# Optimization experiments

Hardware: AMD Instinct MI355X
Metric: run time of the kernel (lower is better)

## Reference

```python
import jax, jax.numpy as jnp
from jax import lax
import numpy as np

WIN_SIZE = 11
WIN_SIGMA = 1.5
DATA_RANGE = 1.0
K1, K2 = 0.01, 0.03
DN = ('NCHW', 'OIHW', 'NCHW')


def _gauss_1d(size, sigma):
    coords = jnp.arange(size, dtype=jnp.float32) - (size // 2)
    g = jnp.exp(-coords ** 2 / (2.0 * sigma ** 2))
    return g / g.sum()


def _gaussian_filter(x, g):
    # depthwise separable valid conv: along W then along H (order irrelevant)
    C = x.shape[1]
    kw = jnp.tile(g.reshape(1, 1, 1, -1), (C, 1, 1, 1))  # [C,1,1,K]
    kh = jnp.tile(g.reshape(1, 1, -1, 1), (C, 1, 1, 1))  # [C,1,K,1]
    x = lax.conv_general_dilated(x, kw, (1, 1), 'VALID',
                                 feature_group_count=C, dimension_numbers=DN)
    x = lax.conv_general_dilated(x, kh, (1, 1), 'VALID',
                                 feature_group_count=C, dimension_numbers=DN)
    return x


def setup_inputs() -> dict:
    key = jax.random.key(0)
    k1, k2 = jax.random.split(key)
    X = jax.random.uniform(k1, (32, 3, 512, 512), dtype=jnp.float32, minval=-1.0, maxval=1.0)
    Y = jax.random.uniform(k2, (32, 3, 512, 512), dtype=jnp.float32, minval=-1.0, maxval=1.0)
    return {"X": X, "Y": Y}


def reference(X, Y):
    # channel == 3 -> normalize from [-1,1] to [0,1]
    X = (X + 1.0) / 2.0
    Y = (Y + 1.0) / 2.0

    g = _gauss_1d(WIN_SIZE, WIN_SIGMA).astype(X.dtype)
    C1 = (K1 * DATA_RANGE) ** 2
    C2 = (K2 * DATA_RANGE) ** 2

    mu1 = _gaussian_filter(X, g)
    mu2 = _gaussian_filter(Y, g)
    mu1_sq = mu1 * mu1
    mu2_sq = mu2 * mu2
    mu1_mu2 = mu1 * mu2

    sigma1_sq = _gaussian_filter(X * X, g) - mu1_sq
    sigma2_sq = _gaussian_filter(Y * Y, g) - mu2_sq
    sigma12 = _gaussian_filter(X * Y, g) - mu1_mu2

    cs_map = (2.0 * sigma12 + C2) / (sigma1_sq + sigma2_sq + C2)
    ssim_map = (2.0 * mu1_mu2 + C1) / (mu1_sq + mu2_sq + C1) * cs_map

    # size_average=True, full=False -> scalar mean SSIM
    return ssim_map.mean()
```

## Files before the change

### kernel.cpp

```cpp
#include <hip/hip_runtime.h>
#include <cmath>


#define HH 512
#define WW 512
#define OH 502
#define OW 502
#define NC 96
#define TXS 32
#define BROWS 32
#define NIT 16
#define RAWR 64
#define RAWP 13
#define HSR 48
#define HP4 33
#define GX 16
#define NSLOT 64

typedef float f4 __attribute__((ext_vector_type(4)));

struct GaussW { float g[11]; };

static __device__ __forceinline__ f4 sp(float s) { return (f4){s, s, s, s}; }

#define FENCE() asm volatile("" ::: "memory")

__global__ __launch_bounds__(256, 4) void ssim_kernel(
        const float* __restrict__ X, const float* __restrict__ Y,
        double* __restrict__ acc, GaussW gw) {
    __shared__ f4 rawS[2 * RAWR * RAWP];
    __shared__ f4 hS[HSR][HP4];
    __shared__ double wsum[4];

    const int tid = threadIdx.x;
    const int C0 = blockIdx.x * TXS;
    const float* Xp = X + (size_t)blockIdx.y * (HH * WW);
    const float* Yp = Y + (size_t)blockIdx.y * (HH * WW);

    auto dma1 = [&](int a, int slot_f4, int row, int c4) {
        const float* bp  = a ? Yp : Xp;
        const float* src = bp + (size_t)min(row, HH - 1) * WW
                              + min(C0 + 4 * c4, WW - 4);
        f4* dst = rawS + a * (RAWR * RAWP) + slot_f4;
        __builtin_amdgcn_global_load_lds(
            (const __attribute__((address_space(1))) void*)src,
            (__attribute__((address_space(3))) void*)dst, 16, 0, 0);
    };

    auto dma_batch = [&](int i) {
        const int half = (i & 1) * (BROWS * RAWP);
        const int br = 32 * i + 42;
        #pragma unroll
        for (int a = 0; a < 2; ++a)
            #pragma unroll
            for (int k = 0; k < 2; ++k) {
                int idx = (k << 8) + tid;
                if (idx < BROWS * RAWP) {
                    int o = idx / 13, c4 = idx - o * 13;
                    dma1(a, half + (k << 8) + (tid & ~63), br + o, c4);
                }
            }
    };

    auto htask = [&](int o, int cg, int rbm, int bm) {
        const int rs = rbm + o;
        int hs = bm + o; if (hs >= HSR) hs -= HSR;
        const int ib = rs * RAWP + cg;
        f4 x0 = rawS[ib + 0], x1 = rawS[ib + 1];
        f4 x2 = rawS[ib + 2], x3 = rawS[ib + 3];
        f4 y0 = rawS[RAWR * RAWP + ib + 0], y1 = rawS[RAWR * RAWP + ib + 1];
        f4 y2 = rawS[RAWR * RAWP + ib + 2], y3 = rawS[RAWR * RAWP + ib + 3];
        float xv[16], yv[16];
        #pragma unroll
        for (int q = 0; q < 4; ++q) {
            xv[q] = x0[q]; xv[4 + q] = x1[q]; xv[8 + q] = x2[q]; xv[12 + q] = x3[q];
            yv[q] = y0[q]; yv[4 + q] = y1[q]; yv[8 + q] = y2[q]; yv[12 + q] = y3[q];
        }
        f4 a0v = sp(0.f), a1v = sp(0.f), a2v = sp(0.f), a3v = sp(0.f);
        #pragma unroll
        for (int k = 0; k < 14; ++k) {
            float x = xv[k], y = yv[k];
            f4 P;
            P.x = x; P.y = y;
            P.z = fmaf(x, x, y * y);
            P.w = x * y;
            #pragma unroll
            for (int j = 0; j < 4; ++j) {
                int u = k - j;
                if (u >= 0 && u < 11) {
                    f4 G = sp(gw.g[u]);
                    if (j == 0) a0v = __builtin_elementwise_fma(G, P, a0v);
                    if (j == 1) a1v = __builtin_elementwise_fma(G, P, a1v);
                    if (j == 2) a2v = __builtin_elementwise_fma(G, P, a2v);
                    if (j == 3) a3v = __builtin_elementwise_fma(G, P, a3v);
                }
            }
        }
        hS[hs][4 * cg + 0] = a0v;
        hS[hs][4 * cg + 1] = a1v;
        hS[hs][4 * cg + 2] = a2v;
        hS[hs][4 * cg + 3] = a3v;
    };

    #pragma unroll
    for (int a = 0; a < 2; ++a)
        #pragma unroll
        for (int k = 0; k < 3; ++k) {
            int idx = (k << 8) + tid;
            if (idx < 42 * RAWP) {
                int o = idx / 13, c4 = idx - o * 13;
                dma1(a, 22 * RAWP + (k << 8) + (tid & ~63), o, c4);
            }
        }
    asm volatile("s_waitcnt vmcnt(0)" ::: "memory");
    __builtin_amdgcn_s_barrier();
    FENCE();

    double tsum = 0.0;
    const int c  = tid & 31;
    const int rb = (tid >> 5) * 4;
    int bm = 0;
    int vb = 0;

    for (int i = 0; i < NIT; ++i) {
        if (i >= 1 && i <= 14) dma_batch(i);

        const int rbm = (i == 0) ? 22 : (((i + 1) & 1) << 5);
        {
            const int cg = (tid >> 3) & 7;
            const int o  = (tid & 7) | ((tid >> 6) << 3);
            htask(o, cg, rbm, bm);
            if (i == 0) {
                if (tid < 64) htask(32 + (tid & 7), (tid >> 3) & 7, rbm, bm);
                if (tid < 16) htask(40 + (tid & 1), (tid >> 1) & 7, rbm, bm);
            }
        }
        asm volatile("s_waitcnt lgkmcnt(0)" ::: "memory");
        __builtin_amdgcn_s_barrier();
        FENCE();
        if (i == 0) dma_batch(0);
        f4 A[4];
        #pragma unroll
        for (int j = 0; j < 4; ++j) A[j] = sp(0.f);
        #pragma unroll
        for (int k = 0; k < 14; ++k) {
            int s = vb + rb + k; if (s >= HSR) s -= HSR;
            f4 v = hS[s][c];
            #pragma unroll
            for (int j = 0; j < 4; ++j) {
                int u = k - j;
                if (u >= 0 && u < 11) {
                    f4 G = sp(gw.g[u]);
                    A[j] = __builtin_elementwise_fma(G, v, A[j]);
                }
            }
        }
        const float C1 = 1.0e-4f;
        const float C2 = 9.0e-4f;
        float nn[4], dd[4];
        #pragma unroll
        for (int j = 0; j < 4; ++j) {
            f4 v = A[j];
            float t1 = v.x + 1.f, t2 = v.y + 1.f;
            float num1 = fmaf(t1 * t2, 0.5f, C1);
            float den1 = fmaf(fmaf(t2, t2, t1 * t1), 0.25f, C1);
            float num2 = fmaf(v.w - v.x * v.y, 0.5f, C2);
            float den2 = fmaf(v.z - fmaf(v.x, v.x, v.y * v.y), 0.25f, C2);
            bool valid = (32 * i + rb + j < OH) & (C0 + c < OW);
            nn[j] = valid ? num1 * num2 : 0.f;
            dd[j] = valid ? den1 * den2 : 1.f;
        }
        float d01 = dd[0] * dd[1], d23 = dd[2] * dd[3];
        float s01 = fmaf(nn[0], dd[1], nn[1] * dd[0]);
        float s23 = fmaf(nn[2], dd[3], nn[3] * dd[2]);
        tsum += (double)(fmaf(s01, d23, s23 * d01) / (d01 * d23));

        asm volatile("s_waitcnt vmcnt(0) lgkmcnt(0)" ::: "memory");
        __builtin_amdgcn_s_barrier();
        FENCE();

        bm = (i == 0) ? 42 : (bm + 32 >= HSR ? bm + 32 - HSR : bm + 32);
        vb = (vb + 32 >= HSR) ? vb + 32 - HSR : vb + 32;
    }

    #pragma unroll
    for (int off = 32; off > 0; off >>= 1)
        tsum += __shfl_down(tsum, off, 64);
    if ((tid & 63) == 0) wsum[tid >> 6] = tsum;
    __syncthreads();
    if (tid == 0) {
        int slot = (blockIdx.x + blockIdx.y * GX) & (NSLOT - 1);
        atomicAdd(&acc[slot * 8], wsum[0] + wsum[1] + wsum[2] + wsum[3]);
    }
}

__global__ void ssim_finalize(const double* __restrict__ acc,
                              float* __restrict__ out) {
    int lane = threadIdx.x;
    double t = acc[lane * 8];
    #pragma unroll
    for (int off = 32; off > 0; off >>= 1)
        t += __shfl_down(t, off, 64);
    if (lane == 0)
        out[0] = (float)(t * (1.0 / (double)((long long)NC * OH * OW)));
}

extern "C" void kernel_launch(void* const* d_in, const int* in_sizes, int n_in,
                              void* d_out, int out_size, void* d_ws, size_t ws_size,
                              hipStream_t stream) {
    const float* X = (const float*)d_in[0];
    const float* Y = (const float*)d_in[1];
    float* out = (float*)d_out;
    double* acc = (double*)d_ws;

    hipMemsetAsync(d_ws, 0, NSLOT * 64, stream);

    GaussW gw;
    {
        double g[11], s = 0.0;
        for (int i = 0; i < 11; ++i) {
            double d = (double)(i - 5);
            g[i] = exp(-d * d / (2.0 * 1.5 * 1.5));
            s += g[i];
        }
        for (int i = 0; i < 11; ++i) gw.g[i] = (float)(g[i] / s);
    }

    dim3 grid(GX, NC);
    ssim_kernel<<<grid, dim3(256), 0, stream>>>(X, Y, acc, gw);
    ssim_finalize<<<1, dim3(64), 0, stream>>>(acc, out);
}
```

Measured before the change: 252.4 us.

## Split image rows across two blocks and shrink raw buffer to ring

```diff
diff --git a/kernel.cpp b/kernel.cpp
--- a/kernel.cpp
+++ b/kernel.cpp
@@ -9,10 +9,10 @@
 #define NC 96
 #define TXS 32
 #define BROWS 32
-#define NIT 16
-#define RAWR 64
-#define RAWP 13
-#define HSR 48
+#define NIT 8
+#define RAWR 48
+#define RAWP 11
+#define HSR 44
 #define HP4 33
 #define GX 16
 #define NSLOT 64
@@ -34,12 +34,13 @@
 
     const int tid = threadIdx.x;
     const int C0 = blockIdx.x * TXS;
-    const float* Xp = X + (size_t)blockIdx.y * (HH * WW);
-    const float* Yp = Y + (size_t)blockIdx.y * (HH * WW);
-
-    auto dma1 = [&](int a, int slot_f4, int row, int c4) {
+    const int R0 = blockIdx.y * (BROWS * NIT);
+    const float* Xp = X + (size_t)blockIdx.z * (HH * WW);
+    const float* Yp = Y + (size_t)blockIdx.z * (HH * WW);
+
+    auto dma1 = [&](int a, int slot_f4, int grow, int c4) {
         const float* bp  = a ? Yp : Xp;
-        const float* src = bp + (size_t)min(row, HH - 1) * WW
+        const float* src = bp + (size_t)min(grow, HH - 1) * WW
                               + min(C0 + 4 * c4, WW - 4);
         f4* dst = rawS + a * (RAWR * RAWP) + slot_f4;
         __builtin_amdgcn_global_load_lds(
@@ -47,24 +48,20 @@
             (__attribute__((address_space(3))) void*)dst, 16, 0, 0);
     };
 
-    auto dma_batch = [&](int i) {
-        const int half = (i & 1) * (BROWS * RAWP);
-        const int br = 32 * i + 42;
-        #pragma unroll
-        for (int a = 0; a < 2; ++a)
-            #pragma unroll
-            for (int k = 0; k < 2; ++k) {
-                int idx = (k << 8) + tid;
-                if (idx < BROWS * RAWP) {
-                    int o = idx / 13, c4 = idx - o * 13;
-                    dma1(a, half + (k << 8) + (tid & ~63), br + o, c4);
-                }
-            }
+    auto dma_half = [&](int i, int h) {
+        const int br = 32 * i + 42 + 16 * h;
+        const int tb = ((br + 6) % RAWR) * RAWP;
+        if (tid < 16 * RAWP) {
+            int o = tid / RAWP, c4 = tid - o * RAWP;
+            int db = tb + (tid & ~63);
+            dma1(0, db, R0 + br + o, c4);
+            dma1(1, db, R0 + br + o, c4);
+        }
     };
 
     auto htask = [&](int o, int cg, int rbm, int bm) {
-        const int rs = rbm + o;
-        int hs = bm + o; if (hs >= HSR) hs -= HSR;
+        int rs = rbm + o; if (rs >= RAWR) rs -= RAWR;
+        int hs = bm + o;  if (hs >= HSR)  hs -= HSR;
         const int ib = rs * RAWP + cg;
         f4 x0 = rawS[ib + 0], x1 = rawS[ib + 1];
         f4 x2 = rawS[ib + 2], x3 = rawS[ib + 3];
@@ -103,15 +100,15 @@
     };
 
     #pragma unroll
-    for (int a = 0; a < 2; ++a)
-        #pragma unroll
-        for (int k = 0; k < 3; ++k) {
-            int idx = (k << 8) + tid;
-            if (idx < 42 * RAWP) {
-                int o = idx / 13, c4 = idx - o * 13;
-                dma1(a, 22 * RAWP + (k << 8) + (tid & ~63), o, c4);
-            }
-        }
+    for (int k = 0; k < 2; ++k) {
+        int idx = (k << 8) + tid;
+        if (idx < 42 * RAWP) {
+            int o = idx / RAWP, c4 = idx - o * RAWP;
+            int db = 6 * RAWP + (k << 8) + (tid & ~63);
+            dma1(0, db, R0 + o, c4);
+            dma1(1, db, R0 + o, c4);
+        }
+    }
     asm volatile("s_waitcnt vmcnt(0)" ::: "memory");
     __builtin_amdgcn_s_barrier();
     FENCE();
@@ -119,13 +116,12 @@
     double tsum = 0.0;
     const int c  = tid & 31;
     const int rb = (tid >> 5) * 4;
-    int bm = 0;
-    int vb = 0;
 
     for (int i = 0; i < NIT; ++i) {
-        if (i >= 1 && i <= 14) dma_batch(i);
-
-        const int rbm = (i == 0) ? 22 : (((i + 1) & 1) << 5);
+        if (i >= 1 && i <= NIT - 2) dma_half(i, 0);
+
+        const int rbm = (i == 0) ? 6 : ((32 * i + 16) % RAWR);
+        const int bm  = (i == 0) ? 0 : ((32 * i + 10) % HSR);
         {
             const int cg = (tid >> 3) & 7;
             const int o  = (tid & 7) | ((tid >> 6) << 3);
@@ -138,7 +134,10 @@
         asm volatile("s_waitcnt lgkmcnt(0)" ::: "memory");
         __builtin_amdgcn_s_barrier();
         FENCE();
-        if (i == 0) dma_batch(0);
+        if (i == 0) dma_half(0, 0);
+        if (i <= NIT - 2) dma_half(i, 1);
+
+        const int vb = (32 * i) % HSR;
         f4 A[4];
         #pragma unroll
         for (int j = 0; j < 4; ++j) A[j] = sp(0.f);
@@ -166,7 +165,7 @@
             float den1 = fmaf(fmaf(t2, t2, t1 * t1), 0.25f, C1);
             float num2 = fmaf(v.w - v.x * v.y, 0.5f, C2);
             float den2 = fmaf(v.z - fmaf(v.x, v.x, v.y * v.y), 0.25f, C2);
-            bool valid = (32 * i + rb + j < OH) & (C0 + c < OW);
+            bool valid = (R0 + 32 * i + rb + j < OH) & (C0 + c < OW);
             nn[j] = valid ? num1 * num2 : 0.f;
             dd[j] = valid ? den1 * den2 : 1.f;
         }
@@ -178,9 +177,6 @@
         asm volatile("s_waitcnt vmcnt(0) lgkmcnt(0)" ::: "memory");
         __builtin_amdgcn_s_barrier();
         FENCE();
-
-        bm = (i == 0) ? 42 : (bm + 32 >= HSR ? bm + 32 - HSR : bm + 32);
-        vb = (vb + 32 >= HSR) ? vb + 32 - HSR : vb + 32;
     }
 
     #pragma unroll
@@ -189,7 +185,8 @@
     if ((tid & 63) == 0) wsum[tid >> 6] = tsum;
     __syncthreads();
     if (tid == 0) {
-        int slot = (blockIdx.x + blockIdx.y * GX) & (NSLOT - 1);
+        int slot = (blockIdx.x + blockIdx.y * GX + blockIdx.z * GX * 2)
+                   & (NSLOT - 1);
         atomicAdd(&acc[slot * 8], wsum[0] + wsum[1] + wsum[2] + wsum[3]);
     }
 }
@@ -226,7 +223,7 @@
         for (int i = 0; i < 11; ++i) gw.g[i] = (float)(g[i] / s);
     }
 
-    dim3 grid(GX, NC);
+    dim3 grid(GX, 2, NC);
     ssim_kernel<<<grid, dim3(256), 0, stream>>>(X, Y, acc, gw);
     ssim_finalize<<<1, dim3(64), 0, stream>>>(acc, out);
 }
```

After: 243.4 us. -3.6%, faster.
